# Performance work log

Measured on AMD Instinct MI355X. Metric: run time of the kernel, lower is better.

## Reference

```python
import jax, jax.numpy as jnp
import numpy as np

EPS = 1e-12      # LayerNorm eps in Selector
TAU = 1e-6       # gumbel-softmax temperature
TOPK = 2         # seg_selector.topk
TOPJ = 128       # reg_selector.topk
NUMC, NUMF_PER_C, NUMP, DIM, QDIM = 4, 4, 256, 1024, 512


def _ln(x, g, b):
    m = x.mean(-1, keepdims=True)
    v = ((x - m) ** 2).mean(-1, keepdims=True)
    return (x - m) / jnp.sqrt(v + EPS) * g + b


def _selector(q, K, V_flat, Wq, bq, ln_q_g, ln_q_b, Wk, bk, ln_k_g, ln_k_b, topk, key):
    # q: (B, qdim); K: (B, n, dim); V_flat: (B, n, F)
    Qp = _ln(q @ Wq.T + bq, ln_q_g, ln_q_b)                      # (B, dim)
    Kp = _ln(K @ Wk.T + bk, ln_k_g, ln_k_b)                      # (B, n, dim)
    probs = jax.nn.softmax(jnp.einsum('bnd,bd->bn', Kp, Qp), axis=-1)  # (B, n)
    B, n = probs.shape
    # F.gumbel_softmax applied to the softmax probs (as in the torch code),
    # vectorized over the topk loop: one mask per selection round.
    u = jax.random.uniform(key, (B, topk, n), minval=1e-20, maxval=1.0)
    g = -jnp.log(-jnp.log(u))
    masks = jax.nn.softmax((probs[:, None, :] + g) / TAU, axis=-1)     # (B, topk, n)
    return jnp.einsum('btn,bnf->btf', masks, V_flat)                   # (B, topk, F)


def setup_inputs() -> dict:
    key = jax.random.key(0)
    ks = jax.random.split(key, 24)
    bz = 8
    s = 0.02
    d = {
        'q_feat': jax.random.normal(ks[0], (bz, QDIM, 1), dtype=jnp.float32),
        'image_embeds': jax.random.normal(ks[1], (bz, NUMC, NUMF_PER_C, NUMP, DIM), dtype=jnp.float32),
        'video_cls': jax.random.normal(ks[2], (bz, NUMC * NUMF_PER_C, DIM), dtype=jnp.float32),
        # seg_selector params
        'seg_Wq': s * jax.random.normal(ks[3], (DIM, QDIM), dtype=jnp.float32),
        'seg_bq': jnp.zeros((DIM,), jnp.float32),
        'seg_ln_q_g': jnp.ones((DIM,), jnp.float32),
        'seg_ln_q_b': jnp.zeros((DIM,), jnp.float32),
        'seg_Wk': s * jax.random.normal(ks[4], (DIM, DIM), dtype=jnp.float32),
        'seg_bk': jnp.zeros((DIM,), jnp.float32),
        'seg_ln_k_g': jnp.ones((DIM,), jnp.float32),
        'seg_ln_k_b': jnp.zeros((DIM,), jnp.float32),
        # reg_selector params
        'reg_Wq': s * jax.random.normal(ks[5], (DIM, QDIM), dtype=jnp.float32),
        'reg_bq': jnp.zeros((DIM,), jnp.float32),
        'reg_ln_q_g': jnp.ones((DIM,), jnp.float32),
        'reg_ln_q_b': jnp.zeros((DIM,), jnp.float32),
        'reg_Wk': s * jax.random.normal(ks[6], (DIM, DIM), dtype=jnp.float32),
        'reg_bk': jnp.zeros((DIM,), jnp.float32),
        'reg_ln_k_g': jnp.ones((DIM,), jnp.float32),
        'reg_ln_k_b': jnp.zeros((DIM,), jnp.float32),
    }
    return d


def reference(q_feat, image_embeds, video_cls,
              seg_Wq, seg_bq, seg_ln_q_g, seg_ln_q_b, seg_Wk, seg_bk, seg_ln_k_g, seg_ln_k_b,
              reg_Wq, reg_bq, reg_ln_q_g, reg_ln_q_b, reg_Wk, reg_bk, reg_ln_k_g, reg_ln_k_b):
    bz = q_feat.shape[0]
    # video_in.view(bz, numc*numf, nump, -1); hdim == dim so no projections
    video_feat = image_embeds.reshape(bz, NUMC * NUMF_PER_C, NUMP, DIM)
    vc = video_cls / jnp.linalg.norm(video_cls, axis=-1, keepdims=True)
    seg_feat = vc.reshape(bz, NUMC, NUMF_PER_C, DIM).mean(axis=2)        # (bz, numc, dim)
    # CLIP text feature, L2-normalized (get_clip_txt_embedding)
    q = q_feat[..., 0]
    q = q / jnp.linalg.norm(q, axis=-1, keepdims=True)                   # (bz, qdim)

    k1, k2 = jax.random.split(jax.random.key(42))
    # seg_selector: K=seg_feat (bz,4,dim), V=video_feat viewed (bz,4, 4*256*1024)
    sel = _selector(q, seg_feat, video_feat.reshape(bz, NUMC, -1),
                    seg_Wq, seg_bq, seg_ln_q_g, seg_ln_q_b,
                    seg_Wk, seg_bk, seg_ln_k_g, seg_ln_k_b, TOPK, k1)
    sel = sel.reshape(bz, TOPK * NUMF_PER_C, NUMP, DIM)                  # (bz, 8, 256, 1024)

    # reg_selector over the flattened pseudo-batch (bz*8)
    B2 = bz * TOPK * NUMF_PER_C
    K2 = sel.reshape(B2, NUMP, DIM)
    q2 = jnp.repeat(q, TOPK * NUMF_PER_C, axis=0)                        # (bz*8, qdim)
    sel2 = _selector(q2, K2, K2, reg_Wq, reg_bq, reg_ln_q_g, reg_ln_q_b,
                     reg_Wk, reg_bk, reg_ln_k_g, reg_ln_k_b, TOPJ, k2)   # (bz*8, 128, 1024)

    return sel2.reshape(bz, 1, TOPK * NUMF_PER_C, TOPJ, DIM)
```

## Files before the change

kernel.cpp:

```cpp
#include <hip/hip_runtime.h>
#include <hip/hip_fp16.h>
#include <stdint.h>

#ifndef JAX_PARTITIONABLE
#define JAX_PARTITIONABLE 1
#endif

typedef _Float16 f16x8 __attribute__((ext_vector_type(8)));
typedef float    f32x4 __attribute__((ext_vector_type(4)));

static constexpr int BZ   = 8;
static constexpr int QD   = 512;
static constexpr int DIM  = 1024;
static constexpr int I2   = 64;
static constexpr int TOPJ = 128;
static constexpr int NROW = 16384;
static constexpr int NCT  = 4;

static constexpr size_t EAI = 0;
static constexpr size_t EWI = (size_t)33554432;
static constexpr size_t FQN   = 17825792;
static constexpr size_t FSF   = FQN + 4096;
static constexpr size_t FYS   = FSF + 32768;
static constexpr size_t FYR   = FYS + 8192;
static constexpr size_t FY2   = FYR + 8192;
static constexpr size_t FGQ   = FY2 + 32768;
static constexpr size_t FSG   = FGQ + 8192;
static constexpr size_t FCL   = FSG + 8;
static constexpr size_t FMS   = FCL + 8;
static constexpr size_t FP2   = FMS + 64;
static constexpr size_t FPART = FP2 + 16384;

__device__ __forceinline__ uint32_t rotl32(uint32_t v, int d){ return (v << d) | (v >> (32 - d)); }

__device__ __forceinline__ void tf2x32(uint32_t k0, uint32_t k1, uint32_t x0, uint32_t x1,
                                       uint32_t& o0, uint32_t& o1){
  const uint32_t ks2 = k0 ^ k1 ^ 0x1BD11BDAu;
  x0 += k0; x1 += k1;
#define TFR(r) x0 += x1; x1 = rotl32(x1, r); x1 ^= x0;
  TFR(13) TFR(15) TFR(26) TFR(6)
  x0 += k1;  x1 += ks2 + 1u;
  TFR(17) TFR(29) TFR(16) TFR(24)
  x0 += ks2; x1 += k0 + 2u;
  TFR(13) TFR(15) TFR(26) TFR(6)
  x0 += k0;  x1 += k1 + 3u;
  TFR(17) TFR(29) TFR(16) TFR(24)
  x0 += k1;  x1 += ks2 + 4u;
  TFR(13) TFR(15) TFR(26) TFR(6)
  x0 += ks2; x1 += k0 + 5u;
#undef TFR
  o0 = x0; o1 = x1;
}

__device__ __forceinline__ void jax_keys(uint32_t& k1a, uint32_t& k1b, uint32_t& k2a, uint32_t& k2b){
#if JAX_PARTITIONABLE
  uint32_t a,b,c,d;
  tf2x32(0u, 42u, 0u, 0u, a, b);
  tf2x32(0u, 42u, 0u, 1u, c, d);
  k1a = a; k1b = b; k2a = c; k2b = d;
#else
  uint32_t a,b,c,d;
  tf2x32(0u, 42u, 0u, 2u, a, b);
  tf2x32(0u, 42u, 1u, 3u, c, d);
  k1a = a; k1b = c; k2a = b; k2b = d;
#endif
}

__device__ __forceinline__ float jax_uniform(uint32_t ka, uint32_t kb, uint32_t idx, uint32_t half_n){
  uint32_t o0, o1, bits;
#if JAX_PARTITIONABLE
  (void)half_n;
  tf2x32(ka, kb, 0u, idx, o0, o1);
  bits = o0 ^ o1;
#else
  if (idx < half_n){ tf2x32(ka, kb, idx, idx + half_n, o0, o1); bits = o0; }
  else             { tf2x32(ka, kb, idx - half_n, idx, o0, o1); bits = o1; }
#endif
  float f = __uint_as_float((bits >> 9) | 0x3f800000u) - 1.0f;
  f = f + 1e-20f;
  return fmaxf(f, 1e-20f);
}

__device__ __forceinline__ float blk_sum(float v, float* red){
  __syncthreads();
  #pragma unroll
  for (int m = 32; m >= 1; m >>= 1) v += __shfl_xor(v, m);
  if ((threadIdx.x & 63) == 0) red[threadIdx.x >> 6] = v;
  __syncthreads();
  return red[0] + red[1] + red[2] + red[3];
}
__device__ __forceinline__ float blk_max(float v, float* red){
  __syncthreads();
  #pragma unroll
  for (int m = 32; m >= 1; m >>= 1) v = fmaxf(v, __shfl_xor(v, m));
  if ((threadIdx.x & 63) == 0) red[threadIdx.x >> 6] = v;
  __syncthreads();
  return fmaxf(fmaxf(red[0], red[1]), fmaxf(red[2], red[3]));
}

__device__ __forceinline__ unsigned short f2h(float x){
  return __half_as_ushort(__float2half(x));
}
__device__ __forceinline__ float h2f(unsigned short u){
  return __half2float(__ushort_as_half(u));
}

__device__ __forceinline__ void gl_lds16(const void* g, void* l){
  __builtin_amdgcn_global_load_lds((const __attribute__((address_space(1))) void*)g,
                                   (__attribute__((address_space(3))) void*)l, 16, 0, 0);
}

__global__ __launch_bounds__(256) void k_matvec(
    const float* __restrict__ qf, const float* __restrict__ vcls,
    const float* __restrict__ sWq, const float* __restrict__ sbq,
    const float* __restrict__ rWq, const float* __restrict__ rbq,
    const float* __restrict__ sWk, const float* __restrict__ sbk,
    float* __restrict__ ws)
{
  const int bid = blockIdx.x;
  const int b = bid >> 5, ch = bid & 31;
  const int tid = threadIdx.x;
  __shared__ float red[4];
  __shared__ float qn[QD];
  __shared__ float sf[4][DIM];

  {
    float q0 = qf[b * QD + tid];
    float q1 = qf[b * QD + 256 + tid];
    float ss = blk_sum(q0*q0 + q1*q1, red);
    float nrm = sqrtf(ss);
    qn[tid] = q0 / nrm;
    qn[tid + 256] = q1 / nrm;
  }
  {
    float sfr[4][4];
    #pragma unroll
    for (int c = 0; c < 4; ++c)
      #pragma unroll
      for (int r = 0; r < 4; ++r) sfr[c][r] = 0.f;
    for (int f = 0; f < 16; ++f){
      float v[4]; float s2 = 0.f;
      #pragma unroll
      for (int r = 0; r < 4; ++r){
        v[r] = vcls[((size_t)(b * 16 + f)) * DIM + tid + (r << 8)];
        s2 += v[r] * v[r];
      }
      float s = blk_sum(s2, red);
      float n2 = sqrtf(s);
      const int c = f >> 2;
      #pragma unroll
      for (int r = 0; r < 4; ++r) sfr[c][r] += v[r] / n2;
    }
    #pragma unroll
    for (int c = 0; c < 4; ++c)
      #pragma unroll
      for (int r = 0; r < 4; ++r)
        sf[c][tid + (r << 8)] = sfr[c][r] * 0.25f;
  }
  __syncthreads();

  const int di = tid >> 3, sub = tid & 7;
  const int d = ch * 32 + di;

  {
    const float* wr = sWq + (size_t)d * QD + sub * 64;
    const float* qq = qn + sub * 64;
    float a = 0.f;
    #pragma unroll
    for (int e = 0; e < 64; e += 4){
      float4 w4 = *(const float4*)(wr + e);
      a += qq[e]*w4.x + qq[e+1]*w4.y + qq[e+2]*w4.z + qq[e+3]*w4.w;
    }
    a += __shfl_xor(a, 1); a += __shfl_xor(a, 2); a += __shfl_xor(a, 4);
    if (sub == 0) ws[FYS + (size_t)b * DIM + d] = a + sbq[d];
  }
  {
    const float* wr = rWq + (size_t)d * QD + sub * 64;
    const float* qq = qn + sub * 64;
    float a = 0.f;
    #pragma unroll
    for (int e = 0; e < 64; e += 4){
      float4 w4 = *(const float4*)(wr + e);
      a += qq[e]*w4.x + qq[e+1]*w4.y + qq[e+2]*w4.z + qq[e+3]*w4.w;
    }
    a += __shfl_xor(a, 1); a += __shfl_xor(a, 2); a += __shfl_xor(a, 4);
    if (sub == 0) ws[FYR + (size_t)b * DIM + d] = a + rbq[d];
  }
  for (int c = 0; c < 4; ++c){
    const float* wr = sWk + (size_t)d * DIM + sub * 128;
    const float* qq = &sf[c][sub * 128];
    float a = 0.f;
    #pragma unroll
    for (int e = 0; e < 128; e += 4){
      float4 w4 = *(const float4*)(wr + e);
      a += qq[e]*w4.x + qq[e+1]*w4.y + qq[e+2]*w4.z + qq[e+3]*w4.w;
    }
    a += __shfl_xor(a, 1); a += __shfl_xor(a, 2); a += __shfl_xor(a, 4);
    if (sub == 0) ws[FY2 + ((size_t)(b * 4 + c)) * DIM + d] = a + sbk[d];
  }
}

__global__ __launch_bounds__(256) void k_post(
    const float* __restrict__ slnqg, const float* __restrict__ slnqb,
    const float* __restrict__ rlnqg, const float* __restrict__ rlnqb,
    const float* __restrict__ rlnkg, const float* __restrict__ rlnkb,
    const float* __restrict__ slnkg, const float* __restrict__ slnkb,
    float* __restrict__ ws)
{
  const int b = blockIdx.x, tid = threadIdx.x;
  __shared__ float red[4];
  __shared__ float qps[DIM];
  __shared__ float lg[4];

  {
    float y[4];
    #pragma unroll
    for (int r = 0; r < 4; ++r) y[r] = ws[FYS + (size_t)b * DIM + tid + (r << 8)];
    float S = blk_sum(y[0]+y[1]+y[2]+y[3], red);
    float mu = S * (1.f / 1024.f);
    float pv = 0.f;
    #pragma unroll
    for (int r = 0; r < 4; ++r){ float dv = y[r]-mu; pv += dv*dv; }
    float V = blk_sum(pv, red);
    float sig = sqrtf(V * (1.f / 1024.f) + 1e-12f);
    #pragma unroll
    for (int r = 0; r < 4; ++r){
      const int d = tid + (r << 8);
      qps[d] = (y[r]-mu)/sig * slnqg[d] + slnqb[d];
    }
  }
  __syncthreads();

  {
    float y[4];
    #pragma unroll
    for (int r = 0; r < 4; ++r) y[r] = ws[FYR + (size_t)b * DIM + tid + (r << 8)];
    float S = blk_sum(y[0]+y[1]+y[2]+y[3], red);
    float mu = S * (1.f / 1024.f);
    float pv = 0.f;
    #pragma unroll
    for (int r = 0; r < 4; ++r){ float dv = y[r]-mu; pv += dv*dv; }
    float V = blk_sum(pv, red);
    float sig = sqrtf(V * (1.f / 1024.f) + 1e-12f);
    float sg = 0.f, cl = 0.f;
    #pragma unroll
    for (int r = 0; r < 4; ++r){
      const int d = tid + (r << 8);
      float o = (y[r]-mu)/sig * rlnqg[d] + rlnqb[d];
      float gv = rlnkg[d] * o;
      ws[FGQ + (size_t)b * DIM + d] = gv;
      sg += gv;
      cl += rlnkb[d] * o;
    }
    float SG = blk_sum(sg, red);
    float CL = blk_sum(cl, red);
    if (tid == 0){ ws[FSG + b] = SG; ws[FCL + b] = CL; }
  }

  for (int c = 0; c < 4; ++c){
    float y[4];
    #pragma unroll
    for (int r = 0; r < 4; ++r) y[r] = ws[FY2 + ((size_t)(b * 4 + c)) * DIM + tid + (r << 8)];
    float S = blk_sum(y[0]+y[1]+y[2]+y[3], red);
    float mu = S * (1.f / 1024.f);
    float pv = 0.f;
    #pragma unroll
    for (int r = 0; r < 4; ++r){ float dv = y[r]-mu; pv += dv*dv; }
    float V = blk_sum(pv, red);
    float sig = sqrtf(V * (1.f / 1024.f) + 1e-12f);
    float lp = 0.f;
    #pragma unroll
    for (int r = 0; r < 4; ++r){
      const int d = tid + (r << 8);
      float kp = (y[r]-mu)/sig * slnkg[d] + slnkb[d];
      lp += kp * qps[d];
    }
    float L = blk_sum(lp, red);
    if (tid == 0) lg[c] = L;
  }
  __syncthreads();

  if (tid == 0){
    float m = fmaxf(fmaxf(lg[0], lg[1]), fmaxf(lg[2], lg[3]));
    float e[4], s = 0.f;
    #pragma unroll
    for (int c = 0; c < 4; ++c){ e[c] = expf(lg[c] - m); s += e[c]; }
    float probs[4];
    #pragma unroll
    for (int c = 0; c < 4; ++c) probs[c] = e[c] / s;
    uint32_t k1a, k1b, k2a, k2b;
    jax_keys(k1a, k1b, k2a, k2b);
    for (int t = 0; t < 2; ++t){
      float x[4];
      #pragma unroll
      for (int c = 0; c < 4; ++c){
        float u = jax_uniform(k1a, k1b, (uint32_t)(b * 8 + t * 4 + c), 32u);
        float gmb = -logf(-logf(u));
        x[c] = (probs[c] + gmb) / 1e-6f;
      }
      float xm = fmaxf(fmaxf(x[0], x[1]), fmaxf(x[2], x[3]));
      float w[4], sw = 0.f;
      #pragma unroll
      for (int c = 0; c < 4; ++c){ w[c] = expf(x[c] - xm); sw += w[c]; }
      #pragma unroll
      for (int c = 0; c < 4; ++c) ws[FMS + b * 8 + t * 4 + c] = w[c] / sw;
    }
  }
}

__global__ __launch_bounds__(256) void k_sel(const float* __restrict__ E,
                                             const float* __restrict__ W,
                                             float* __restrict__ ws)
{
  const int blk = blockIdx.x;
  const int th = threadIdx.x;
  const int kc = th >> 3;
  const int c  = (th & 7) >> 1;
  const int pos = (th & 1) * 4;
  const int d = th << 2;

  if (blk < 2048){
    const int r0 = blk * 8;
    const int i = r0 >> 8;
    const int bz = i >> 3, it = i & 7, t = it >> 2, j = it & 3;
    const int p0 = r0 & 255;
    const float* msk = ws + FMS + bz * 8 + t * 4;

    float4 a[8];
    #pragma unroll
    for (int r = 0; r < 8; ++r) a[r] = (float4){0.f, 0.f, 0.f, 0.f};

    #pragma unroll
    for (int cc = 0; cc < 4; ++cc){
      const float w = msk[cc];
      if (w != 0.f){
        const float* ep = E + (((size_t)((bz * 4 + cc) * 4 + j)) * 256 + p0) * DIM + d;
        #pragma unroll
        for (int r = 0; r < 8; ++r){
          const float4 v = *(const float4*)(ep + (size_t)r * DIM);
          a[r].x = fmaf(w, v.x, a[r].x);
          a[r].y = fmaf(w, v.y, a[r].y);
          a[r].z = fmaf(w, v.z, a[r].z);
          a[r].w = fmaf(w, v.w, a[r].w);
        }
      }
    }
    unsigned short* AI = (unsigned short*)ws + EAI;
    #pragma unroll
    for (int r = 0; r < 8; ++r){
      ushort4 h, l;
      h.x = f2h(a[r].x); l.x = f2h(a[r].x - h2f(h.x));
      h.y = f2h(a[r].y); l.y = f2h(a[r].y - h2f(h.y));
      h.z = f2h(a[r].z); l.z = f2h(a[r].z - h2f(h.z));
      h.w = f2h(a[r].w); l.w = f2h(a[r].w - h2f(h.w));
      const size_t base = (size_t)(r0 + r) * 2048 + kc * 64;
      *(ushort4*)&AI[base + c * 8 + pos]      = h;
      *(ushort4*)&AI[base + c * 8 + pos + 32] = l;
    }
  } else {
    const int r0 = (blk - 2048) * 8;
    unsigned short* WI = (unsigned short*)ws + EWI;
    float4 v[8];
    #pragma unroll
    for (int r = 0; r < 8; ++r)
      v[r] = *(const float4*)&W[(size_t)(r0 + r) * DIM + d];
    #pragma unroll
    for (int r = 0; r < 8; ++r){
      ushort4 h, l;
      h.x = f2h(v[r].x); l.x = f2h(v[r].x - h2f(h.x));
      h.y = f2h(v[r].y); l.y = f2h(v[r].y - h2f(h.y));
      h.z = f2h(v[r].z); l.z = f2h(v[r].z - h2f(h.z));
      h.w = f2h(v[r].w); l.w = f2h(v[r].w - h2f(h.w));
      const size_t base = (size_t)(r0 + r) * 2048 + kc * 64;
      *(ushort4*)&WI[base + c * 8 + pos]      = h;
      *(ushort4*)&WI[base + c * 8 + pos + 32] = l;
    }
  }
}

__global__ __launch_bounds__(512) void k_gemm(const float* __restrict__ bk,
                                              float* __restrict__ ws)
{
  const unsigned short* AI = (const unsigned short*)ws + EAI;
  const unsigned short* WI = (const unsigned short*)ws + EWI;
  const float* gq = ws + FGQ;
  float* part = ws + FPART;

  __shared__ __align__(16) unsigned short Abuf[2][16384];
  __shared__ __align__(16) unsigned short Bbuf[2][16384];

  const int bid = blockIdx.x;
  const int xcd = bid & 7, g = bid >> 3;
  const int rt = xcd * 8 + (g >> 2);
  const int ct = g & 3;
  const int R0 = rt * 256, C0 = ct * 256;
  const int tid = threadIdx.x;
  const int lane = tid & 63, wid = tid >> 6;
  const int wr = wid >> 2, wc = wid & 3;
  const int b = R0 >> 11;

  const int src_off = (lane >> 3) * 2048 + (((lane & 7) ^ (lane >> 3)) << 3);
  const int pcH = ((lane >> 4) ^ (lane & 7)) * 16;
  const int pcL = pcH ^ 64;
  const int raw = wr * 128 + (lane & 15);
  const int rbw = wc * 64 + (lane & 15);

  f32x4 acc[8][4];
  #pragma unroll
  for (int m = 0; m < 8; ++m)
    #pragma unroll
    for (int n = 0; n < 4; ++n)
      acc[m][n] = (f32x4){0.f, 0.f, 0.f, 0.f};

  auto stageA = [&](int buf, int kc){
    const unsigned short* As = AI + (size_t)(R0 + wid * 32) * 2048 + kc * 64 + src_off;
    unsigned short* Ad = &Abuf[buf][wid * 2048];
    #pragma unroll
    for (int q = 0; q < 4; ++q) gl_lds16(As + (size_t)q * 8 * 2048, Ad + q * 512);
  };
  auto stageB = [&](int buf, int kc){
    const unsigned short* Bs = WI + (size_t)(C0 + wid * 32) * 2048 + kc * 64 + src_off;
    unsigned short* Bd = &Bbuf[buf][wid * 2048];
    #pragma unroll
    for (int q = 0; q < 4; ++q) gl_lds16(Bs + (size_t)q * 8 * 2048, Bd + q * 512);
  };

  stageA(0, 0);
  stageB(0, 0);
  asm volatile("s_waitcnt vmcnt(0)" ::: "memory");
  __builtin_amdgcn_s_barrier();

  f16x8 ah[4], al[4], bh[4], bl[4];

  #pragma unroll 1
  for (int kc = 0; kc < 32; ++kc){
    const int cur = kc & 1;
    const char* pa = (const char*)&Abuf[cur][0];
    const char* pb = (const char*)&Bbuf[cur][0];

    #pragma unroll
    for (int f = 0; f < 4; ++f){
      const int ro = (raw + f * 16) << 7;
      ah[f] = *(const f16x8*)(pa + ro + pcH);
      al[f] = *(const f16x8*)(pa + ro + pcL);
    }
    #pragma unroll
    for (int f = 0; f < 2; ++f){
      const int ro = (rbw + f * 16) << 7;
      bh[f] = *(const f16x8*)(pb + ro + pcH);
      bl[f] = *(const f16x8*)(pb + ro + pcL);
    }
    if (kc < 31) stageA(cur ^ 1, kc + 1);
    asm volatile("s_waitcnt lgkmcnt(0)" ::: "memory");
    __builtin_amdgcn_sched_barrier(0);
    __builtin_amdgcn_s_setprio(1);
    #pragma unroll
    for (int m = 0; m < 4; ++m)
      #pragma unroll
      for (int n = 0; n < 2; ++n){
        acc[m][n] = __builtin_amdgcn_mfma_f32_16x16x32_f16(ah[m], bh[n], acc[m][n], 0, 0, 0);
        acc[m][n] = __builtin_amdgcn_mfma_f32_16x16x32_f16(ah[m], bl[n], acc[m][n], 0, 0, 0);
        acc[m][n] = __builtin_amdgcn_mfma_f32_16x16x32_f16(al[m], bh[n], acc[m][n], 0, 0, 0);
      }
    __builtin_amdgcn_s_setprio(0);

    #pragma unroll
    for (int f = 2; f < 4; ++f){
      const int ro = (rbw + f * 16) << 7;
      bh[f] = *(const f16x8*)(pb + ro + pcH);
      bl[f] = *(const f16x8*)(pb + ro + pcL);
    }
    if (kc < 31) stageB(cur ^ 1, kc + 1);
    asm volatile("s_waitcnt lgkmcnt(0)" ::: "memory");
    __builtin_amdgcn_sched_barrier(0);
    __builtin_amdgcn_s_setprio(1);
    #pragma unroll
    for (int m = 0; m < 4; ++m)
      #pragma unroll
      for (int n = 2; n < 4; ++n){
        acc[m][n] = __builtin_amdgcn_mfma_f32_16x16x32_f16(ah[m], bh[n], acc[m][n], 0, 0, 0);
        acc[m][n] = __builtin_amdgcn_mfma_f32_16x16x32_f16(ah[m], bl[n], acc[m][n], 0, 0, 0);
        acc[m][n] = __builtin_amdgcn_mfma_f32_16x16x32_f16(al[m], bh[n], acc[m][n], 0, 0, 0);
      }
    __builtin_amdgcn_s_setprio(0);

    #pragma unroll
    for (int f = 0; f < 4; ++f){
      const int ro = (raw + 64 + f * 16) << 7;
      ah[f] = *(const f16x8*)(pa + ro + pcH);
      al[f] = *(const f16x8*)(pa + ro + pcL);
    }
    asm volatile("s_waitcnt lgkmcnt(0)" ::: "memory");
    __builtin_amdgcn_sched_barrier(0);
    __builtin_amdgcn_s_setprio(1);
    #pragma unroll
    for (int m = 0; m < 4; ++m)
      #pragma unroll
      for (int n = 0; n < 2; ++n){
        acc[m + 4][n] = __builtin_amdgcn_mfma_f32_16x16x32_f16(ah[m], bh[n], acc[m + 4][n], 0, 0, 0);
        acc[m + 4][n] = __builtin_amdgcn_mfma_f32_16x16x32_f16(ah[m], bl[n], acc[m + 4][n], 0, 0, 0);
        acc[m + 4][n] = __builtin_amdgcn_mfma_f32_16x16x32_f16(al[m], bh[n], acc[m + 4][n], 0, 0, 0);
      }
    __builtin_amdgcn_s_setprio(0);

    __builtin_amdgcn_s_setprio(1);
    #pragma unroll
    for (int m = 0; m < 4; ++m)
      #pragma unroll
      for (int n = 2; n < 4; ++n){
        acc[m + 4][n] = __builtin_amdgcn_mfma_f32_16x16x32_f16(ah[m], bh[n], acc[m + 4][n], 0, 0, 0);
        acc[m + 4][n] = __builtin_amdgcn_mfma_f32_16x16x32_f16(ah[m], bl[n], acc[m + 4][n], 0, 0, 0);
        acc[m + 4][n] = __builtin_amdgcn_mfma_f32_16x16x32_f16(al[m], bh[n], acc[m + 4][n], 0, 0, 0);
      }
    __builtin_amdgcn_s_setprio(0);
    asm volatile("s_waitcnt lgkmcnt(0)" ::: "memory");
    __builtin_amdgcn_sched_barrier(0);
    asm volatile("s_waitcnt vmcnt(0)" ::: "memory");
    __builtin_amdgcn_s_barrier();
  }

  float bkv[4], gv[4];
  #pragma unroll
  for (int n = 0; n < 4; ++n){
    const int col = C0 + wc * 64 + n * 16 + (lane & 15);
    bkv[n] = bk[col];
    gv[n]  = gq[(size_t)b * DIM + col];
  }
  float* fred = (float*)&Abuf[0][0];
  #pragma unroll
  for (int m = 0; m < 8; ++m)
    #pragma unroll
    for (int r = 0; r < 4; ++r){
      float s = 0.f, q = 0.f, tv = 0.f;
      #pragma unroll
      for (int n = 0; n < 4; ++n){
        float y = acc[m][n][r] + bkv[n];
        s += y; q += y * y; tv += y * gv[n];
      }
      #pragma unroll
      for (int msk = 8; msk >= 1; msk >>= 1){
        s += __shfl_xor(s, msk); q += __shfl_xor(q, msk); tv += __shfl_xor(tv, msk);
      }
      if ((lane & 15) == 0){
        const int rl = wr * 128 + m * 16 + (lane >> 4) * 4 + r;
        fred[(rl * 4 + wc) * 3 + 0] = s;
        fred[(rl * 4 + wc) * 3 + 1] = q;
        fred[(rl * 4 + wc) * 3 + 2] = tv;
      }
    }
  __syncthreads();
  if (tid < 256){
    #pragma unroll
    for (int st = 0; st < 3; ++st){
      float v = fred[(tid * 4 + 0) * 3 + st] + fred[(tid * 4 + 1) * 3 + st]
              + fred[(tid * 4 + 2) * 3 + st] + fred[(tid * 4 + 3) * 3 + st];
      part[((size_t)ct * NROW + R0 + tid) * 3 + st] = v;
    }
  }
}

__global__ __launch_bounds__(256) void k_out(const float* __restrict__ E,
                                             const float* __restrict__ ws,
                                             float* __restrict__ out)
{
  const int bid = blockIdx.x;
  const int i = bid >> 7, t2 = bid & 127;
  const int bz = i >> 3, it = i & 7, tt = it >> 2, j = it & 3;
  const int tid = threadIdx.x;
  __shared__ float red[4];
  __shared__ float wv[256];
  __shared__ float mloc[4];
  __shared__ unsigned long long mk[4];

  if (tid < 4) mloc[tid] = ws[FMS + bz * 8 + tt * 4 + tid];

  const float* part = ws + FPART;
  const int r = i * 256 + tid;
  float S = 0.f, Q = 0.f, T = 0.f;
  #pragma unroll
  for (int ct = 0; ct < NCT; ++ct){
    const float* pp = part + ((size_t)ct * NROW + r) * 3;
    S += pp[0]; Q += pp[1]; T += pp[2];
  }
  float mu  = S * (1.f / 1024.f);
  float var = Q * (1.f / 1024.f) - mu * mu;
  float sig = sqrtf(var + 1e-12f);
  float L = (T - mu * ws[FSG + bz]) / sig + ws[FCL + bz];
  float ML = blk_max(L, red);
  float wp2 = expf(L - ML);
  float swp = blk_sum(wp2, red);
  float p2 = wp2 / swp;

  uint32_t k1a, k1b, k2a, k2b;
  jax_keys(k1a, k1b, k2a, k2b);
  const uint32_t fidx = ((uint32_t)(i * TOPJ + t2)) * 256u + (uint32_t)tid;
  float u = jax_uniform(k2a, k2b, fidx, 1048576u);
  float gmb = -logf(-logf(u));
  float x = (p2 + gmb) / 1e-6f;
  float M = blk_max(x, red);
  float w = expf(x - M);
  float sw = blk_sum(w, red);
  float wn = w / sw;
  wv[tid] = wn;
  unsigned long long bal = __ballot(wn != 0.f);
  if ((tid & 63) == 0) mk[tid >> 6] = bal;
  __syncthreads();

  const int d = tid << 2;
  float4 acc = {0.f, 0.f, 0.f, 0.f};
  for (int wq = 0; wq < 4; ++wq){
    unsigned long long mm = mk[wq];
    while (mm){
      const int l = __ffsll(mm) - 1;
      mm &= mm - 1;
      const int p = (wq << 6) + l;
      const float wpv = wv[p];
      #pragma unroll
      for (int c = 0; c < 4; ++c){
        const float mc = mloc[c];
        if (mc != 0.f){
          const float4 v = *(const float4*)&E[(((size_t)((bz * 4 + c) * 4 + j)) * 256 + p) * DIM + d];
          const float wm = wpv * mc;
          acc.x += wm * v.x; acc.y += wm * v.y; acc.z += wm * v.z; acc.w += wm * v.w;
        }
      }
    }
  }
  *(float4*)&out[((size_t)(i * TOPJ + t2)) * DIM + d] = acc;
}

extern "C" void kernel_launch(void* const* d_in, const int* in_sizes, int n_in,
                              void* d_out, int out_size, void* d_ws, size_t ws_size,
                              hipStream_t stream)
{
  const float* qf    = (const float*)d_in[0];
  const float* E     = (const float*)d_in[1];
  const float* vcls  = (const float*)d_in[2];
  const float* sWq   = (const float*)d_in[3];
  const float* sbq   = (const float*)d_in[4];
  const float* slnqg = (const float*)d_in[5];
  const float* slnqb = (const float*)d_in[6];
  const float* sWk   = (const float*)d_in[7];
  const float* sbk   = (const float*)d_in[8];
  const float* slnkg = (const float*)d_in[9];
  const float* slnkb = (const float*)d_in[10];
  const float* rWq   = (const float*)d_in[11];
  const float* rbq   = (const float*)d_in[12];
  const float* rlnqg = (const float*)d_in[13];
  const float* rlnqb = (const float*)d_in[14];
  const float* rWk   = (const float*)d_in[15];
  const float* rbk   = (const float*)d_in[16];
  const float* rlnkg = (const float*)d_in[17];
  const float* rlnkb = (const float*)d_in[18];
  float* ws  = (float*)d_ws;
  float* out = (float*)d_out;

  k_matvec<<<256, 256, 0, stream>>>(qf, vcls, sWq, sbq, rWq, rbq, sWk, sbk, ws);
  k_post<<<BZ, 256, 0, stream>>>(slnqg, slnqb, rlnqg, rlnqb, rlnkg, rlnkb, slnkg, slnkb, ws);
  k_sel<<<2176, 256, 0, stream>>>(E, rWk, ws);
  k_gemm<<<256, 512, 0, stream>>>(rbk, ws);
  k_out<<<I2 * TOPJ, 256, 0, stream>>>(E, ws, out);
}
```

Baseline: 164.4 us.

## Software-pipeline A-fragment LDS reads row by row with MFMA groups

Restructures the inner k-loop of the split-fp16 GEMM. All B fragments are loaded up front, and A fragments are read in double-buffered pairs so each 16-row MFMA group overlaps the LDS read of the next row. Both global-to-LDS stages are issued together early in the iteration, and the explicit lgkmcnt waits between phases are removed in favour of sched_barriers. This aims to hide LDS latency and lower A-register pressure, but it relies on the compiler inserting correct waits and could raise B-register pressure.

```diff
diff --git a/kernel.cpp b/kernel.cpp
--- a/kernel.cpp
+++ b/kernel.cpp
@@ -430,7 +430,25 @@
   asm volatile("s_waitcnt vmcnt(0)" ::: "memory");
   __builtin_amdgcn_s_barrier();
 
-  f16x8 ah[4], al[4], bh[4], bl[4];
+#define READ_PAIR(H, L, FM) do {                       \
+    const int ro_ = (raw + (FM) * 16) << 7;            \
+    (H) = *(const f16x8*)(pa + ro_ + pcH);             \
+    (L) = *(const f16x8*)(pa + ro_ + pcL);             \
+  } while (0)
+
+#define MFMA_ROW(M, H, L) do {                                                           \
+    __builtin_amdgcn_s_setprio(1);                                                       \
+    _Pragma("unroll")                                                                    \
+    for (int n = 0; n < 4; ++n){                                                         \
+      acc[M][n] = __builtin_amdgcn_mfma_f32_16x16x32_f16((H), bh[n], acc[M][n], 0, 0, 0); \
+      acc[M][n] = __builtin_amdgcn_mfma_f32_16x16x32_f16((H), bl[n], acc[M][n], 0, 0, 0); \
+      acc[M][n] = __builtin_amdgcn_mfma_f32_16x16x32_f16((L), bh[n], acc[M][n], 0, 0, 0); \
+    }                                                                                    \
+    __builtin_amdgcn_s_setprio(0);                                                       \
+    __builtin_amdgcn_sched_barrier(0);                                                   \
+  } while (0)
+
+  f16x8 aeh, ael, aoh, aol, bh[4], bl[4];
 
   #pragma unroll 1
   for (int kc = 0; kc < 32; ++kc){
@@ -440,84 +458,44 @@
 
     #pragma unroll
     for (int f = 0; f < 4; ++f){
-      const int ro = (raw + f * 16) << 7;
-      ah[f] = *(const f16x8*)(pa + ro + pcH);
-      al[f] = *(const f16x8*)(pa + ro + pcL);
-    }
-    #pragma unroll
-    for (int f = 0; f < 2; ++f){
       const int ro = (rbw + f * 16) << 7;
       bh[f] = *(const f16x8*)(pb + ro + pcH);
       bl[f] = *(const f16x8*)(pb + ro + pcL);
     }
-    if (kc < 31) stageA(cur ^ 1, kc + 1);
-    asm volatile("s_waitcnt lgkmcnt(0)" ::: "memory");
-    __builtin_amdgcn_sched_barrier(0);
-    __builtin_amdgcn_s_setprio(1);
-    #pragma unroll
-    for (int m = 0; m < 4; ++m)
-      #pragma unroll
-      for (int n = 0; n < 2; ++n){
-        acc[m][n] = __builtin_amdgcn_mfma_f32_16x16x32_f16(ah[m], bh[n], acc[m][n], 0, 0, 0);
-        acc[m][n] = __builtin_amdgcn_mfma_f32_16x16x32_f16(ah[m], bl[n], acc[m][n], 0, 0, 0);
-        acc[m][n] = __builtin_amdgcn_mfma_f32_16x16x32_f16(al[m], bh[n], acc[m][n], 0, 0, 0);
-      }
-    __builtin_amdgcn_s_setprio(0);
-
-    #pragma unroll
-    for (int f = 2; f < 4; ++f){
-      const int ro = (rbw + f * 16) << 7;
-      bh[f] = *(const f16x8*)(pb + ro + pcH);
-      bl[f] = *(const f16x8*)(pb + ro + pcL);
-    }
-    if (kc < 31) stageB(cur ^ 1, kc + 1);
-    asm volatile("s_waitcnt lgkmcnt(0)" ::: "memory");
-    __builtin_amdgcn_sched_barrier(0);
-    __builtin_amdgcn_s_setprio(1);
-    #pragma unroll
-    for (int m = 0; m < 4; ++m)
-      #pragma unroll
-      for (int n = 2; n < 4; ++n){
-        acc[m][n] = __builtin_amdgcn_mfma_f32_16x16x32_f16(ah[m], bh[n], acc[m][n], 0, 0, 0);
-        acc[m][n] = __builtin_amdgcn_mfma_f32_16x16x32_f16(ah[m], bl[n], acc[m][n], 0, 0, 0);
-        acc[m][n] = __builtin_amdgcn_mfma_f32_16x16x32_f16(al[m], bh[n], acc[m][n], 0, 0, 0);
-      }
-    __builtin_amdgcn_s_setprio(0);
-
-    #pragma unroll
-    for (int f = 0; f < 4; ++f){
-      const int ro = (raw + 64 + f * 16) << 7;
-      ah[f] = *(const f16x8*)(pa + ro + pcH);
-      al[f] = *(const f16x8*)(pa + ro + pcL);
-    }
-    asm volatile("s_waitcnt lgkmcnt(0)" ::: "memory");
-    __builtin_amdgcn_sched_barrier(0);
-    __builtin_amdgcn_s_setprio(1);
-    #pragma unroll
-    for (int m = 0; m < 4; ++m)
-      #pragma unroll
-      for (int n = 0; n < 2; ++n){
-        acc[m + 4][n] = __builtin_amdgcn_mfma_f32_16x16x32_f16(ah[m], bh[n], acc[m + 4][n], 0, 0, 0);
-        acc[m + 4][n] = __builtin_amdgcn_mfma_f32_16x16x32_f16(ah[m], bl[n], acc[m + 4][n], 0, 0, 0);
-        acc[m + 4][n] = __builtin_amdgcn_mfma_f32_16x16x32_f16(al[m], bh[n], acc[m + 4][n], 0, 0, 0);
-      }
-    __builtin_amdgcn_s_setprio(0);
-
-    __builtin_amdgcn_s_setprio(1);
-    #pragma unroll
-    for (int m = 0; m < 4; ++m)
-      #pragma unroll
-      for (int n = 2; n < 4; ++n){
-        acc[m + 4][n] = __builtin_amdgcn_mfma_f32_16x16x32_f16(ah[m], bh[n], acc[m + 4][n], 0, 0, 0);
-        acc[m + 4][n] = __builtin_amdgcn_mfma_f32_16x16x32_f16(ah[m], bl[n], acc[m + 4][n], 0, 0, 0);
-        acc[m + 4][n] = __builtin_amdgcn_mfma_f32_16x16x32_f16(al[m], bh[n], acc[m + 4][n], 0, 0, 0);
-      }
-    __builtin_amdgcn_s_setprio(0);
+    READ_PAIR(aeh, ael, 0);
+    READ_PAIR(aoh, aol, 1);
+    __builtin_amdgcn_sched_barrier(0);
+    if (kc < 31){ stageA(cur ^ 1, kc + 1); stageB(cur ^ 1, kc + 1); }
+    __builtin_amdgcn_sched_barrier(0);
+
+    MFMA_ROW(0, aeh, ael);
+    READ_PAIR(aeh, ael, 2);
+    __builtin_amdgcn_sched_barrier(0);
+    MFMA_ROW(1, aoh, aol);
+    READ_PAIR(aoh, aol, 3);
+    __builtin_amdgcn_sched_barrier(0);
+    MFMA_ROW(2, aeh, ael);
+    READ_PAIR(aeh, ael, 4);
+    __builtin_amdgcn_sched_barrier(0);
+    MFMA_ROW(3, aoh, aol);
+    READ_PAIR(aoh, aol, 5);
+    __builtin_amdgcn_sched_barrier(0);
+    MFMA_ROW(4, aeh, ael);
+    READ_PAIR(aeh, ael, 6);
+    __builtin_amdgcn_sched_barrier(0);
+    MFMA_ROW(5, aoh, aol);
+    READ_PAIR(aoh, aol, 7);
+    __builtin_amdgcn_sched_barrier(0);
+    MFMA_ROW(6, aeh, ael);
+    MFMA_ROW(7, aoh, aol);
+
     asm volatile("s_waitcnt lgkmcnt(0)" ::: "memory");
     __builtin_amdgcn_sched_barrier(0);
     asm volatile("s_waitcnt vmcnt(0)" ::: "memory");
     __builtin_amdgcn_s_barrier();
   }
+#undef READ_PAIR
+#undef MFMA_ROW
 
   float bkv[4], gv[4];
   #pragma unroll
```

Measured after the change: 169.1 us. 2.8% more time.
